# Performance work log

Measured on AMD Instinct MI355X. Metric: run time of the kernel, lower is better.

Reference implementation:

```python
import jax, jax.numpy as jnp
import numpy as np

EPS = 1e-12  # matches torch F.normalize default eps

def setup_inputs() -> dict:
    key = jax.random.key(0)
    k1, k2 = jax.random.split(key)
    n_verts, n_faces = 1000000, 2000000
    v = jax.random.normal(k1, (n_verts, 3), dtype=jnp.float32)
    faces = jax.random.randint(k2, (n_faces, 3), 0, n_verts, dtype=jnp.int32)
    return {"v": v, "faces": faces}

def reference(v, faces):
    # gather triangle vertices: [n_faces, 3, 3]
    tri = v[faces]
    v0, v1, v2 = tri[:, 0, :], tri[:, 1, :], tri[:, 2, :]
    e0 = v1 - v0
    e1 = v2 - v1
    e2 = v0 - v2
    face_normals = (jnp.cross(e0, e1) + jnp.cross(e1, e2) + jnp.cross(e2, e0))  # [n_faces, 3]
    # scatter-add each face normal to its 3 vertices (unsorted_segment_sum over f)
    vn = jnp.zeros_like(v).at[faces].add(face_normals[:, None, :])  # [n_verts, 3]
    norm = jnp.linalg.norm(vn, axis=-1, keepdims=True)
    vn = vn / jnp.maximum(norm, EPS)
    return vn
```

## Files before the change

kernel.cpp:

```cpp
#include <hip/hip_runtime.h>

#define VN_EPS 1e-12f
#define VB_SHIFT 12
#define VB 4096
#define NBP 256
#define FB 1536
#define FPB_MAX 1312
#define REC_MAX 3936
#define QBIAS 33554432u
#define QSCALE 8192.0f
#define QINV 1.220703125e-4f

__device__ __forceinline__ void face_normal(
    float v0x, float v0y, float v0z,
    float v1x, float v1y, float v1z,
    float v2x, float v2y, float v2z,
    float& nx, float& ny, float& nz) {
    float e0x = v1x - v0x, e0y = v1y - v0y, e0z = v1z - v0z;
    float e1x = v2x - v1x, e1y = v2y - v1y, e1z = v2z - v1z;
    float e2x = v0x - v2x, e2y = v0y - v2y, e2z = v0z - v2z;
    nx = (e0y * e1z - e0z * e1y) + (e1y * e2z - e1z * e2y) + (e2y * e0z - e2z * e0y);
    ny = (e0z * e1x - e0x * e1z) + (e1z * e2x - e1x * e2z) + (e2z * e0x - e2x * e0z);
    nz = (e0x * e1y - e0y * e1x) + (e1x * e2y - e1y * e2x) + (e2x * e0y - e2y * e0x);
}

__device__ __forceinline__ void face_normal_from_verts(
    const float* __restrict__ v, int i0, int i1, int i2,
    float& nx, float& ny, float& nz) {
    face_normal(v[3 * i0], v[3 * i0 + 1], v[3 * i0 + 2],
                v[3 * i1], v[3 * i1 + 1], v[3 * i1 + 2],
                v[3 * i2], v[3 * i2 + 1], v[3 * i2 + 2], nx, ny, nz);
}

__device__ __forceinline__ void encode_rec(float nx, float ny, float nz,
                                           unsigned lidx,
                                           unsigned& w0, unsigned& w1) {
    float m = fmaxf(fabsf(nx), fmaxf(fabsf(ny), fabsf(nz)));
    int ee = (int)(__float_as_uint(m) >> 23) - 127;
    ee = min(max(ee, -21), 10);
    float scale = __uint_as_float((unsigned)((140 - ee) << 23));
    int qx = __float2int_rn(nx * scale);
    int qy = __float2int_rn(ny * scale);
    int qz = __float2int_rn(nz * scale);
    qx = min(max(qx, -16383), 16383);
    qy = min(max(qy, -16383), 16383);
    qz = min(max(qz, -16383), 16383);
    unsigned eb = (unsigned)(ee + 21);
    w0 = ((unsigned)qx & 0x7fffu) | (((unsigned)qy & 0x7fffu) << 15);
    w1 = ((unsigned)qz & 0x7fffu) | (eb << 15) | (lidx << 20);
}

__device__ __forceinline__ uint2 encode_vert(float x, float y, float z) {
    float cx = fminf(fmaxf(x, -7.99999f), 7.99999f);
    float cy = fminf(fmaxf(y, -7.99999f), 7.99999f);
    float cz = fminf(fmaxf(z, -7.99999f), 7.99999f);
    unsigned ux = (unsigned)__float2uint_rn((cx + 8.0f) * 131072.0f) & 0x1FFFFFu;
    unsigned uy = (unsigned)__float2uint_rn((cy + 8.0f) * 131072.0f) & 0x1FFFFFu;
    unsigned uz = (unsigned)__float2uint_rn((cz + 8.0f) * 131072.0f) & 0x1FFFFFu;
    return make_uint2(ux | (uy << 21), (uy >> 11) | (uz << 10));
}

__device__ __forceinline__ void decode_vert(uint2 w, float& x, float& y, float& z) {
    unsigned ux = w.x & 0x1FFFFFu;
    unsigned uy = (w.x >> 21) | ((w.y & 0x3FFu) << 11);
    unsigned uz = (w.y >> 10) & 0x1FFFFFu;
    const float k = 7.62939453125e-06f;
    x = fmaf((float)ux, k, -8.0f);
    y = fmaf((float)uy, k, -8.0f);
    z = fmaf((float)uz, k, -8.0f);
}

__global__ void __launch_bounds__(512) vn_vconv(const float* __restrict__ v,
                                                uint2* __restrict__ vq,
                                                int n_verts) {
    int i = blockIdx.x * blockDim.x + threadIdx.x;
    if (i >= n_verts) return;
    vq[i] = encode_vert(v[3 * i + 0], v[3 * i + 1], v[3 * i + 2]);
}

__global__ void __launch_bounds__(256) vn_count(const int* __restrict__ faces,
                                                unsigned* __restrict__ cnt_counts,
                                                int n_faces, int fpb) {
    __shared__ unsigned h[NBP];
    for (int k = threadIdx.x; k < NBP; k += 256) h[k] = 0;
    __syncthreads();
    int fbeg = blockIdx.x * fpb;
    int fend = min(fbeg + fpb, n_faces);
    for (int f = fbeg + (int)threadIdx.x; f < fend; f += 256) {
        int i0 = __builtin_nontemporal_load(&faces[3 * f + 0]);
        int i1 = __builtin_nontemporal_load(&faces[3 * f + 1]);
        int i2 = __builtin_nontemporal_load(&faces[3 * f + 2]);
        atomicAdd(&h[(unsigned)i0 >> VB_SHIFT], 1u);
        atomicAdd(&h[(unsigned)i1 >> VB_SHIFT], 1u);
        atomicAdd(&h[(unsigned)i2 >> VB_SHIFT], 1u);
    }
    __syncthreads();
    unsigned* row = cnt_counts + (size_t)blockIdx.x * NBP;
    for (int k = threadIdx.x; k < NBP; k += 256) row[k] = h[k];
}

__global__ void __launch_bounds__(256) vn_scan_blocks(const unsigned* __restrict__ cnt_counts,
                                                      unsigned* __restrict__ cnt_scan,
                                                      unsigned* __restrict__ bb) {
    int b = blockIdx.x;
    int t = threadIdx.x;
    unsigned v[6];
    unsigned csum = 0;
    #pragma unroll
    for (int j = 0; j < 6; ++j) {
        unsigned x = cnt_counts[(size_t)(t * 6 + j) * NBP + b];
        v[j] = csum;
        csum += x;
    }
    __shared__ unsigned s[256];
    s[t] = csum;
    __syncthreads();
    for (int off = 1; off < 256; off <<= 1) {
        unsigned x = (t >= off) ? s[t - off] : 0;
        __syncthreads();
        s[t] += x;
        __syncthreads();
    }
    unsigned excl = s[t] - csum;
    #pragma unroll
    for (int j = 0; j < 6; ++j)
        cnt_scan[(size_t)(t * 6 + j) * NBP + b] = excl + v[j];
    if (t == 255) bb[b] = s[255];
}

__global__ void __launch_bounds__(256) vn_scan_buckets(unsigned* __restrict__ bb, int NB) {
    int t = threadIdx.x;
    __shared__ unsigned s[256];
    unsigned mine = (t < NB) ? bb[t] : 0;
    s[t] = mine;
    __syncthreads();
    for (int off = 1; off < 256; off <<= 1) {
        unsigned x = (t >= off) ? s[t - off] : 0;
        __syncthreads();
        s[t] += x;
        __syncthreads();
    }
    if (t < NB) bb[t] = s[t] - mine;
    if (t == 255) bb[NB] = s[255];
}

__global__ void __launch_bounds__(512)
vn_fill(const uint2* __restrict__ vq,
        const int* __restrict__ faces,
        const unsigned* __restrict__ cnt_counts,
        const unsigned* __restrict__ cnt_scan,
        const unsigned* __restrict__ bb,
        unsigned long long* __restrict__ rec,
        int n_faces, int fpb, int NB) {
    __shared__ unsigned s_seg[NBP];
    __shared__ unsigned s_cur[NBP];
    __shared__ unsigned s_gbase[NBP];
    __shared__ unsigned s_r0[REC_MAX];
    __shared__ unsigned s_r1[REC_MAX];

    int tid = threadIdx.x;
    const unsigned* crow = cnt_counts + (size_t)blockIdx.x * NBP;
    const unsigned* srow = cnt_scan + (size_t)blockIdx.x * NBP;

    {
        unsigned own = 0;
        if (tid < NBP) {
            own = crow[tid];
            s_seg[tid] = own;
            s_gbase[tid] = (tid < NB) ? (srow[tid] + bb[tid]) : 0u;
        }
        __syncthreads();
        for (int off = 1; off < NBP; off <<= 1) {
            unsigned y = 0;
            if (tid < NBP && tid >= off) y = s_seg[tid - off];
            __syncthreads();
            if (tid < NBP) s_seg[tid] += y;
            __syncthreads();
        }
        if (tid < NBP) {
            unsigned excl = s_seg[tid] - own;
            s_seg[tid] = excl;
            s_cur[tid] = excl;
        }
        __syncthreads();
    }

    int fbeg = blockIdx.x * fpb;
    int fend = min(fbeg + fpb, n_faces);

    {
        int fa[3];
        bool m[3];
        #pragma unroll
        for (int s = 0; s < 3; ++s) {
            int f = fbeg + tid + s * 512;
            m[s] = f < fend;
            fa[s] = m[s] ? f : fbeg;
        }
        if (fend > fbeg) {
            int i0[3], i1[3], i2[3];
            #pragma unroll
            for (int s = 0; s < 3; ++s) {
                i0[s] = __builtin_nontemporal_load(&faces[3 * fa[s] + 0]);
                i1[s] = __builtin_nontemporal_load(&faces[3 * fa[s] + 1]);
                i2[s] = __builtin_nontemporal_load(&faces[3 * fa[s] + 2]);
            }
            uint2 w0v[3], w1v[3], w2v[3];
            #pragma unroll
            for (int s = 0; s < 3; ++s) {
                w0v[s] = vq[i0[s]];
                w1v[s] = vq[i1[s]];
                w2v[s] = vq[i2[s]];
            }
            #pragma unroll
            for (int s = 0; s < 3; ++s) {
                if (m[s]) {
                    float x0, y0, z0, x1, y1, z1, x2, y2, z2;
                    decode_vert(w0v[s], x0, y0, z0);
                    decode_vert(w1v[s], x1, y1, z1);
                    decode_vert(w2v[s], x2, y2, z2);
                    float nx, ny, nz;
                    face_normal(x0, y0, z0, x1, y1, z1, x2, y2, z2, nx, ny, nz);
                    int idx3[3] = {i0[s], i1[s], i2[s]};
                    #pragma unroll
                    for (int j = 0; j < 3; ++j) {
                        unsigned idx = (unsigned)idx3[j];
                        unsigned b = idx >> VB_SHIFT;
                        unsigned w0, w1;
                        encode_rec(nx, ny, nz, idx & (VB - 1), w0, w1);
                        unsigned slot = atomicAdd(&s_cur[b], 1u);
                        s_r0[slot] = w0;
                        s_r1[slot] = w1;
                    }
                }
            }
        }
    }
    __syncthreads();

    int T = 3 * (fend - fbeg);
    for (int k = tid; k < T; k += 512) {
        unsigned w0 = s_r0[k], w1 = s_r1[k];
        int lo2 = 0, hi2 = NBP - 1;
        #pragma unroll
        for (int it = 0; it < 8; ++it) {
            int mid = (lo2 + hi2 + 1) >> 1;
            bool ge = (s_seg[mid] <= (unsigned)k);
            lo2 = ge ? mid : lo2;
            hi2 = ge ? hi2 : mid - 1;
        }
        unsigned b = (unsigned)lo2;
        unsigned dst = s_gbase[b] + ((unsigned)k - s_seg[b]);
        unsigned long long w = ((unsigned long long)w1 << 32) | w0;
        __builtin_nontemporal_store(w, &rec[dst]);
    }
}

__global__ void __launch_bounds__(1024) vn_reduce_norm(const unsigned* __restrict__ bb,
                                                       const unsigned long long* __restrict__ rec,
                                                       float* __restrict__ out,
                                                       int n_verts) {
    __shared__ unsigned long long acc[VB * 2];
    for (int k = threadIdx.x; k < VB * 2; k += 1024) acc[k] = 0ull;
    __syncthreads();
    int b = blockIdx.x;
    unsigned beg = bb[b], end = bb[b + 1];

    unsigned e = beg + threadIdx.x;
    for (; e + 7u * 1024u < end; e += 8u * 1024u) {
        unsigned long long w[8];
        #pragma unroll
        for (int j = 0; j < 8; ++j) w[j] = __builtin_nontemporal_load(&rec[e + (unsigned)j * 1024u]);
        #pragma unroll
        for (int j = 0; j < 8; ++j) {
            unsigned w0 = (unsigned)w[j], w1 = (unsigned)(w[j] >> 32);
            int qx = ((int)(w0 << 17)) >> 17;
            int qy = ((int)(w0 << 2)) >> 17;
            int qz = ((int)(w1 << 17)) >> 17;
            unsigned eb = (w1 >> 15) & 31u;
            unsigned li = w1 >> 20;
            float sc = __uint_as_float((eb + 93u) << 23) * QSCALE;
            int fx = __float2int_rn((float)qx * sc);
            int fy = __float2int_rn((float)qy * sc);
            int fz = __float2int_rn((float)qz * sc);
            fx = min(max(fx, -16777216), 16777216);
            fy = min(max(fy, -16777216), 16777216);
            fz = min(max(fz, -16777216), 16777216);
            unsigned long long a = ((unsigned long long)(unsigned)(fy + (int)QBIAS) << 32)
                                 | (unsigned)(fx + (int)QBIAS);
            unsigned long long c = (1ull << 32) | (unsigned)(fz + (int)QBIAS);
            atomicAdd(&acc[2 * li + 0], a);
            atomicAdd(&acc[2 * li + 1], c);
        }
    }
    for (; e < end; e += 1024u) {
        unsigned long long wf = __builtin_nontemporal_load(&rec[e]);
        unsigned w0 = (unsigned)wf, w1 = (unsigned)(wf >> 32);
        int qx = ((int)(w0 << 17)) >> 17;
        int qy = ((int)(w0 << 2)) >> 17;
        int qz = ((int)(w1 << 17)) >> 17;
        unsigned eb = (w1 >> 15) & 31u;
        unsigned li = w1 >> 20;
        float sc = __uint_as_float((eb + 93u) << 23) * QSCALE;
        int fx = __float2int_rn((float)qx * sc);
        int fy = __float2int_rn((float)qy * sc);
        int fz = __float2int_rn((float)qz * sc);
        fx = min(max(fx, -16777216), 16777216);
        fy = min(max(fy, -16777216), 16777216);
        fz = min(max(fz, -16777216), 16777216);
        unsigned long long a = ((unsigned long long)(unsigned)(fy + (int)QBIAS) << 32)
                             | (unsigned)(fx + (int)QBIAS);
        unsigned long long c = (1ull << 32) | (unsigned)(fz + (int)QBIAS);
        atomicAdd(&acc[2 * li + 0], a);
        atomicAdd(&acc[2 * li + 1], c);
    }
    __syncthreads();

    int vbase = b << VB_SHIFT;
    for (int k = threadIdx.x; k < VB; k += 1024) {
        int i = vbase + k;
        if (i < n_verts) {
            unsigned long long a = acc[2 * k + 0];
            unsigned long long c = acc[2 * k + 1];
            unsigned cnt = (unsigned)(c >> 32);
            int sx = (int)((unsigned)a - cnt * QBIAS);
            int sy = (int)((unsigned)(a >> 32) - cnt * QBIAS);
            int sz = (int)((unsigned)c - cnt * QBIAS);
            float x = (float)sx * QINV;
            float y = (float)sy * QINV;
            float z = (float)sz * QINV;
            float n = sqrtf(x * x + y * y + z * z);
            float inv = 1.0f / fmaxf(n, VN_EPS);
            out[3 * (size_t)i + 0] = x * inv;
            out[3 * (size_t)i + 1] = y * inv;
            out[3 * (size_t)i + 2] = z * inv;
        }
    }
}

__global__ void vn_face_scatter(const float* __restrict__ v,
                                const int* __restrict__ faces,
                                float* __restrict__ vn,
                                int n_faces) {
    int f = blockIdx.x * blockDim.x + threadIdx.x;
    if (f >= n_faces) return;
    int i0 = faces[3 * f + 0];
    int i1 = faces[3 * f + 1];
    int i2 = faces[3 * f + 2];
    float nx, ny, nz;
    face_normal_from_verts(v, i0, i1, i2, nx, ny, nz);
    atomicAdd(&vn[3 * i0 + 0], nx);
    atomicAdd(&vn[3 * i0 + 1], ny);
    atomicAdd(&vn[3 * i0 + 2], nz);
    atomicAdd(&vn[3 * i1 + 0], nx);
    atomicAdd(&vn[3 * i1 + 1], ny);
    atomicAdd(&vn[3 * i1 + 2], nz);
    atomicAdd(&vn[3 * i2 + 0], nx);
    atomicAdd(&vn[3 * i2 + 1], ny);
    atomicAdd(&vn[3 * i2 + 2], nz);
}

__global__ void vn_normalize(float* __restrict__ vn, int n_verts) {
    int i = blockIdx.x * blockDim.x + threadIdx.x;
    if (i >= n_verts) return;
    float x = vn[3 * i + 0];
    float y = vn[3 * i + 1];
    float z = vn[3 * i + 2];
    float n = sqrtf(x * x + y * y + z * z);
    float inv = 1.0f / fmaxf(n, VN_EPS);
    vn[3 * i + 0] = x * inv;
    vn[3 * i + 1] = y * inv;
    vn[3 * i + 2] = z * inv;
}

extern "C" void kernel_launch(void* const* d_in, const int* in_sizes, int n_in,
                              void* d_out, int out_size, void* d_ws, size_t ws_size,
                              hipStream_t stream) {
    const float* v = (const float*)d_in[0];
    const int* faces = (const int*)d_in[1];
    float* vn = (float*)d_out;

    int n_verts = in_sizes[0] / 3;
    int n_faces = in_sizes[1] / 3;

    int NB = (n_verts + VB - 1) >> VB_SHIFT;
    size_t n_contrib = 3 * (size_t)n_faces;
    int fpb = (n_faces + FB - 1) / FB;

    size_t sz_cnt = (size_t)FB * NBP * 4;
    size_t off_scan = sz_cnt;
    size_t off_bb = off_scan + sz_cnt;
    size_t off_vq = off_bb + 4096;
    size_t sz_vq = ((size_t)n_verts * 8 + 255) & ~(size_t)255;
    size_t off_rec = off_vq + sz_vq;
    size_t need = off_rec + 8 * n_contrib;

    if (NB <= NBP && fpb <= FPB_MAX && ws_size >= need) {
        unsigned* cnt_counts = (unsigned*)d_ws;
        unsigned* cnt_scan = (unsigned*)((char*)d_ws + off_scan);
        unsigned* bb = (unsigned*)((char*)d_ws + off_bb);
        uint2* vq = (uint2*)((char*)d_ws + off_vq);
        unsigned long long* rec = (unsigned long long*)((char*)d_ws + off_rec);

        vn_vconv<<<(n_verts + 511) / 512, 512, 0, stream>>>(v, vq, n_verts);
        vn_count<<<FB, 256, 0, stream>>>(faces, cnt_counts, n_faces, fpb);
        vn_scan_blocks<<<NB, 256, 0, stream>>>(cnt_counts, cnt_scan, bb);
        vn_scan_buckets<<<1, 256, 0, stream>>>(bb, NB);
        vn_fill<<<FB, 512, 0, stream>>>(vq, faces, cnt_counts, cnt_scan, bb, rec,
                                        n_faces, fpb, NB);
        vn_reduce_norm<<<NB, 1024, 0, stream>>>(bb, rec, vn, n_verts);
    } else {
        hipMemsetAsync(vn, 0, (size_t)out_size * sizeof(float), stream);
        vn_face_scatter<<<(n_faces + 255) / 256, 256, 0, stream>>>(v, faces, vn, n_faces);
        vn_normalize<<<(n_verts + 255) / 256, 256, 0, stream>>>(vn, n_verts);
    }
}
```

Baseline: 123.5 us.

## Merge vertex encode and face histogram kernels; drop nontemporal loads/stores

Fuses the vertex quantization kernel and the per-block bucket count kernel into one launch, with extra blocks handling vertex encoding. This removes a launch and lets both independent streaming jobs overlap. Separately, it replaces the nontemporal loads and stores on faces and the record buffer with ordinary accesses, so faces read in the count pass can stay cached for the fill pass and records written in fill can be reused by the reduce pass. The risk is cache pollution and a mixed-role kernel with uneven block workloads.

```diff
diff --git a/kernel.cpp b/kernel.cpp
--- a/kernel.cpp
+++ b/kernel.cpp
@@ -7,6 +7,7 @@
 #define FB 1536
 #define FPB_MAX 1312
 #define REC_MAX 3936
+#define VPB 2048
 #define QBIAS 33554432u
 #define QSCALE 8192.0f
 #define QINV 1.220703125e-4f
@@ -70,33 +71,36 @@
     z = fmaf((float)uz, k, -8.0f);
 }
 
-__global__ void __launch_bounds__(512) vn_vconv(const float* __restrict__ v,
-                                                uint2* __restrict__ vq,
-                                                int n_verts) {
-    int i = blockIdx.x * blockDim.x + threadIdx.x;
-    if (i >= n_verts) return;
-    vq[i] = encode_vert(v[3 * i + 0], v[3 * i + 1], v[3 * i + 2]);
-}
-
-__global__ void __launch_bounds__(256) vn_count(const int* __restrict__ faces,
-                                                unsigned* __restrict__ cnt_counts,
-                                                int n_faces, int fpb) {
-    __shared__ unsigned h[NBP];
-    for (int k = threadIdx.x; k < NBP; k += 256) h[k] = 0;
-    __syncthreads();
-    int fbeg = blockIdx.x * fpb;
-    int fend = min(fbeg + fpb, n_faces);
-    for (int f = fbeg + (int)threadIdx.x; f < fend; f += 256) {
-        int i0 = __builtin_nontemporal_load(&faces[3 * f + 0]);
-        int i1 = __builtin_nontemporal_load(&faces[3 * f + 1]);
-        int i2 = __builtin_nontemporal_load(&faces[3 * f + 2]);
-        atomicAdd(&h[(unsigned)i0 >> VB_SHIFT], 1u);
-        atomicAdd(&h[(unsigned)i1 >> VB_SHIFT], 1u);
-        atomicAdd(&h[(unsigned)i2 >> VB_SHIFT], 1u);
-    }
-    __syncthreads();
-    unsigned* row = cnt_counts + (size_t)blockIdx.x * NBP;
-    for (int k = threadIdx.x; k < NBP; k += 256) row[k] = h[k];
+__global__ void __launch_bounds__(256) vn_prep(const float* __restrict__ v,
+                                               const int* __restrict__ faces,
+                                               unsigned* __restrict__ cnt_counts,
+                                               uint2* __restrict__ vq,
+                                               int n_verts, int n_faces, int fpb) {
+    if (blockIdx.x < FB) {
+        __shared__ unsigned h[NBP];
+        for (int k = threadIdx.x; k < NBP; k += 256) h[k] = 0;
+        __syncthreads();
+        int fbeg = blockIdx.x * fpb;
+        int fend = min(fbeg + fpb, n_faces);
+        for (int f = fbeg + (int)threadIdx.x; f < fend; f += 256) {
+            int i0 = faces[3 * f + 0];
+            int i1 = faces[3 * f + 1];
+            int i2 = faces[3 * f + 2];
+            atomicAdd(&h[(unsigned)i0 >> VB_SHIFT], 1u);
+            atomicAdd(&h[(unsigned)i1 >> VB_SHIFT], 1u);
+            atomicAdd(&h[(unsigned)i2 >> VB_SHIFT], 1u);
+        }
+        __syncthreads();
+        unsigned* row = cnt_counts + (size_t)blockIdx.x * NBP;
+        for (int k = threadIdx.x; k < NBP; k += 256) row[k] = h[k];
+    } else {
+        int vb = blockIdx.x - FB;
+        int beg = vb * VPB;
+        int end = min(beg + VPB, n_verts);
+        for (int i = beg + (int)threadIdx.x; i < end; i += 256) {
+            vq[i] = encode_vert(v[3 * i + 0], v[3 * i + 1], v[3 * i + 2]);
+        }
+    }
 }
 
 __global__ void __launch_bounds__(256) vn_scan_blocks(const unsigned* __restrict__ cnt_counts,
@@ -201,9 +205,9 @@
             int i0[3], i1[3], i2[3];
             #pragma unroll
             for (int s = 0; s < 3; ++s) {
-                i0[s] = __builtin_nontemporal_load(&faces[3 * fa[s] + 0]);
-                i1[s] = __builtin_nontemporal_load(&faces[3 * fa[s] + 1]);
-                i2[s] = __builtin_nontemporal_load(&faces[3 * fa[s] + 2]);
+                i0[s] = faces[3 * fa[s] + 0];
+                i1[s] = faces[3 * fa[s] + 1];
+                i2[s] = faces[3 * fa[s] + 2];
             }
             uint2 w0v[3], w1v[3], w2v[3];
             #pragma unroll
@@ -251,8 +255,7 @@
         }
         unsigned b = (unsigned)lo2;
         unsigned dst = s_gbase[b] + ((unsigned)k - s_seg[b]);
-        unsigned long long w = ((unsigned long long)w1 << 32) | w0;
-        __builtin_nontemporal_store(w, &rec[dst]);
+        rec[dst] = ((unsigned long long)w1 << 32) | w0;
     }
 }
 
@@ -270,7 +273,7 @@
     for (; e + 7u * 1024u < end; e += 8u * 1024u) {
         unsigned long long w[8];
         #pragma unroll
-        for (int j = 0; j < 8; ++j) w[j] = __builtin_nontemporal_load(&rec[e + (unsigned)j * 1024u]);
+        for (int j = 0; j < 8; ++j) w[j] = rec[e + (unsigned)j * 1024u];
         #pragma unroll
         for (int j = 0; j < 8; ++j) {
             unsigned w0 = (unsigned)w[j], w1 = (unsigned)(w[j] >> 32);
@@ -294,7 +297,7 @@
         }
     }
     for (; e < end; e += 1024u) {
-        unsigned long long wf = __builtin_nontemporal_load(&rec[e]);
+        unsigned long long wf = rec[e];
         unsigned w0 = (unsigned)wf, w1 = (unsigned)(wf >> 32);
         int qx = ((int)(w0 << 17)) >> 17;
         int qy = ((int)(w0 << 2)) >> 17;
@@ -402,12 +405,13 @@
         uint2* vq = (uint2*)((char*)d_ws + off_vq);
         unsigned long long* rec = (unsigned long long*)((char*)d_ws + off_rec);
 
-        vn_vconv<<<(n_verts + 511) / 512, 512, 0, stream>>>(v, vq, n_verts);
-        vn_count<<<FB, 256, 0, stream>>>(faces, cnt_counts, n_faces, fpb);
+        int vcb = (n_verts + VPB - 1) / VPB;
+        vn_prep<<<FB + vcb, 256, 0, stream>>>(v, faces, cnt_counts, vq,
+                                              n_verts, n_faces, fpb);
         vn_scan_blocks<<<NB, 256, 0, stream>>>(cnt_counts, cnt_scan, bb);
         vn_scan_buckets<<<1, 256, 0, stream>>>(bb, NB);
-        vn_fill<<<FB, 512, 0, stream>>>(vq, faces, cnt_counts, cnt_scan, bb, rec,
-                                        n_faces, fpb, NB);
+        vn_fill<<<FB, 512, 0, stream>>>(vq, faces, cnt_counts, cnt_scan, bb,
+                                        rec, n_faces, fpb, NB);
         vn_reduce_norm<<<NB, 1024, 0, stream>>>(bb, rec, vn, n_verts);
     } else {
         hipMemsetAsync(vn, 0, (size_t)out_size * sizeof(float), stream);
```

After: 116.0 us. -6.1%, faster.
